# Performance work log

Hardware: AMD Instinct MI355X
Metric: run time of the kernel (lower is better)

## Reference

```python
import jax, jax.numpy as jnp
import numpy as np


def _conv(x, w):
    # stride-2, pad-1, 3x3 conv, NCHW activations, HWIO kernel
    return jax.lax.conv_general_dilated(
        x, w, (2, 2), [(1, 1), (1, 1)],
        dimension_numbers=('NCHW', 'HWIO', 'NCHW'))


def setup_inputs() -> dict:
    key = jax.random.key(0)
    ks = iter(jax.random.split(key, 40))
    def rn(shape, scale=1.0):
        return jax.random.normal(next(ks), shape, jnp.float32) * scale
    d = {}
    d['img'] = rn((64, 3, 128, 128))
    d['qst'] = rn((64, 128))
    d['conv_w0'] = rn((3, 3, 3, 24), 1.0 / np.sqrt(3 * 9))
    for i in (1, 2, 3):
        d['conv_w%d' % i] = rn((3, 3, 24, 24), 1.0 / np.sqrt(24 * 9))
    for i in range(4):
        d['bn_s%d' % i] = jax.random.uniform(next(ks), (24,), jnp.float32, 0.5, 1.5)
        d['bn_b%d' % i] = rn((24,), 0.1)
    d['g_w1'] = rn((180, 256), 1.0 / np.sqrt(180))
    d['g_b1'] = rn((256,), 0.01)
    for i in (2, 3, 4):
        d['g_w%d' % i] = rn((256, 256), 1.0 / np.sqrt(256))
        d['g_b%d' % i] = rn((256,), 0.01)
    d['f_w1'] = rn((256, 256), 1.0 / np.sqrt(256))
    d['f_b1'] = rn((256,), 0.01)
    d['f_w2'] = rn((256, 256), 1.0 / np.sqrt(256))
    d['f_b2'] = rn((256,), 0.01)
    d['cls_w'] = rn((256, 32), 1.0 / np.sqrt(256))
    d['cls_b'] = rn((32,), 0.01)
    return d


def reference(img, qst, conv_w0, conv_w1, conv_w2, conv_w3,
              bn_s0, bn_b0, bn_s1, bn_b1, bn_s2, bn_b2, bn_s3, bn_b3,
              g_w1, g_b1, g_w2, g_b2, g_w3, g_b3, g_w4, g_b4,
              f_w1, f_b1, f_w2, f_b2, cls_w, cls_b):
    x = img
    for w, s, b in ((conv_w0, bn_s0, bn_b0), (conv_w1, bn_s1, bn_b1),
                    (conv_w2, bn_s2, bn_b2), (conv_w3, bn_s3, bn_b3)):
        x = jax.nn.relu(_conv(x, w) * s[None, :, None, None] + b[None, :, None, None])
    N, C, H, W = x.shape  # [64, 24, 8, 8]
    # positional encoding: coords_x, coords_y in [-1,1]
    cx, cy = jnp.meshgrid(jnp.linspace(-1.0, 1.0, W), jnp.linspace(-1.0, 1.0, H))
    pos = jnp.broadcast_to(jnp.stack([cx, cy])[None], (N, 2, H, W)).astype(x.dtype)
    x = jnp.concatenate([x, pos], axis=1)              # [N, C+2, H, W]
    Cf = C + 2
    x = x.transpose(0, 2, 3, 1).reshape(N, H * W, Cf)  # [N, HW, 26]
    # RN_G first linear decomposed over concat([x_i, x_j, qst]) so the huge
    # [N, HW, HW, 2C+q] concat tensor is never materialized (same math).
    W1a, W1b, W1c = g_w1[:Cf], g_w1[Cf:2 * Cf], g_w1[2 * Cf:]
    hi = x @ W1a                      # [N, HW, 256]
    hj = x @ W1b                      # [N, HW, 256]
    hq = qst @ W1c + g_b1             # [N, 256]
    h = jax.nn.relu(hi[:, :, None, :] + hj[:, None, :, :] + hq[:, None, None, :])  # [N,HW,HW,256]
    h = jax.nn.relu(h @ g_w2 + g_b2)
    h = jax.nn.relu(h @ g_w3 + g_b3)
    h = jax.nn.relu(h @ g_w4 + g_b4)
    s = h.sum(axis=(1, 2))            # sum over all HW*HW pairs -> [N, 256]
    # RN_F (dropout is identity in eval mode)
    y = jax.nn.relu(s @ f_w1 + f_b1)
    y = jax.nn.relu(y @ f_w2 + f_b2)
    return jax.nn.log_softmax(y @ cls_w + cls_b, axis=1)
```

## Files before the change

### kernel.cpp

```cpp
#include <hip/hip_runtime.h>
#include <hip/hip_bf16.h>
#include <math.h>

typedef __bf16 bf16x8 __attribute__((ext_vector_type(8)));
typedef __bf16 bf16x4 __attribute__((ext_vector_type(4)));
typedef float  f32x4  __attribute__((ext_vector_type(4)));

#define LH 264

__device__ __host__ inline int fperm(int p) {
  return (p & 0xC0) | ((p & 0x0C) << 2) | ((p >> 2) & 0x0C) | (p & 3);
}

__global__ __launch_bounds__(256) void k1(const float* __restrict__ img, const float* __restrict__ w0,
    const float* __restrict__ bs0, const float* __restrict__ bb0,
    const float* __restrict__ g2, const float* __restrict__ g3, const float* __restrict__ g4,
    const float* __restrict__ gw1, const float* __restrict__ gb1, const float* __restrict__ qst,
    float* __restrict__ c0, __bf16* __restrict__ Wt, float* __restrict__ hq,
    float* __restrict__ sbuf) {
  __shared__ __align__(16) float smem[8224];
  const int blk = blockIdx.x, t = threadIdx.x;

  if (blk < 512) {
    float* wl = smem;
    for (int i = t; i < 648; i += 256) wl[i] = w0[i];
    __syncthreads();
    const int H = 128, W = 128;
    int idx = blk * 256 + t;
    int oxh = idx & 31; int tt = idx >> 5; int oy = tt & 63; int n = tt >> 6;
    int ox0 = oxh * 2;
    float acc0[24], acc1[24];
#pragma unroll
    for (int co = 0; co < 24; ++co) { acc0[co] = 0.f; acc1[co] = 0.f; }
    for (int ci = 0; ci < 3; ++ci) {
      const float* xp = img + (size_t)(n * 3 + ci) * H * W;
#pragma unroll
      for (int ky = 0; ky < 3; ++ky) {
        int iy = 2 * oy + ky - 1;
        if (iy < 0 || iy >= H) continue;
        const float* row = xp + (size_t)iy * W;
        int ixb = 2 * ox0 - 1;
        float in[7];
#pragma unroll
        for (int u = 0; u < 7; ++u) {
          int ix = ixb + u;
          in[u] = (ix >= 0 && ix < W) ? row[ix] : 0.f;
        }
#pragma unroll
        for (int kx = 0; kx < 3; ++kx) {
          const float* wp = &wl[((ky * 3 + kx) * 3 + ci) * 24];
          float v0 = in[kx], v1 = in[kx + 2];
#pragma unroll
          for (int co = 0; co < 24; ++co) {
            float wv = wp[co];
            acc0[co] += v0 * wv;
            acc1[co] += v1 * wv;
          }
        }
      }
    }
    float* yp = c0 + ((size_t)((n * 64 + oy) * 64) + ox0) * 24;
#pragma unroll
    for (int v = 0; v < 6; ++v) {
      f32x4 o;
#pragma unroll
      for (int j = 0; j < 4; ++j) {
        int co = v * 4 + j;
        o[j] = fmaxf(acc0[co] * bs0[co] + bb0[co], 0.f);
      }
      *(f32x4*)(yp + v * 4) = o;
    }
#pragma unroll
    for (int v = 0; v < 6; ++v) {
      f32x4 o;
#pragma unroll
      for (int j = 0; j < 4; ++j) {
        int co = v * 4 + j;
        o[j] = fmaxf(acc1[co] * bs0[co] + bb0[co], 0.f);
      }
      *(f32x4*)(yp + 24 + v * 4) = o;
    }
  } else if (blk < 536) {
    float* tile = smem;
    const int lb = blk - 512;
    const int l = lb >> 3, ks = lb & 7;
    const float* src = (l == 0) ? g2 : (l == 1) ? g3 : g4;
    for (int kk = 0; kk < 32; ++kk) tile[kk * 257 + t] = src[(ks * 32 + kk) * 256 + t];
    __syncthreads();
    const int q = t & 3, nb = t >> 2;
    __bf16* out = Wt + (size_t)(l * 8 + ks) * 8192;
#pragma unroll
    for (int i = 0; i < 4; ++i) {
      int nn = i * 64 + nb;
      int fsel = (l < 2) ? fperm(nn) : nn;
      bf16x8 v;
#pragma unroll
      for (int j = 0; j < 8; ++j) v[j] = (__bf16)tile[(q * 8 + j) * 257 + fsel];
      *(bf16x8*)&out[nn * 32 + q * 8] = v;
    }
  } else {
    float* qs = smem;
    const int n = blk - 536;
    sbuf[n * 256 + t] = 0.f;
    if (t < 128) qs[t] = qst[n * 128 + t];
    __syncthreads();
    float a = gb1[t];
    for (int c = 0; c < 128; ++c) a += qs[c] * gw1[(52 + c) * 256 + t];
    hq[n * 256 + t] = a;
  }
}

__global__ __launch_bounds__(256) void conv1_k(const float* __restrict__ x, const float* __restrict__ w,
                                               const float* __restrict__ sc, const float* __restrict__ bi,
                                               float* __restrict__ y) {
  __shared__ __align__(16) float wl[5184];
  const int t = threadIdx.x;
  for (int i = t; i < 5184; i += 256) wl[i] = w[i];
  __syncthreads();
  int idx = blockIdx.x * 256 + t;
  int ox = idx & 31, oy = (idx >> 5) & 31, n = idx >> 10;
  f32x4 acc4[6];
#pragma unroll
  for (int v = 0; v < 6; ++v) acc4[v] = (f32x4){0.f, 0.f, 0.f, 0.f};
  const float* xb = x + (size_t)n * 4096 * 24;
#pragma unroll
  for (int ky = 0; ky < 3; ++ky) {
    int iy = 2 * oy + ky - 1;
    if (iy < 0 || iy >= 64) continue;
#pragma unroll
    for (int kx = 0; kx < 3; ++kx) {
      int ix = 2 * ox + kx - 1;
      if (ix < 0 || ix >= 64) continue;
      const float* xp = xb + (size_t)(iy * 64 + ix) * 24;
      const float* wt = &wl[((ky * 3 + kx) * 24) * 24];
      for (int c4 = 0; c4 < 6; ++c4) {
        f32x4 xq = *(const f32x4*)(xp + c4 * 4);
        const float* wb4 = wt + (c4 * 4) * 24;
#pragma unroll
        for (int j = 0; j < 4; ++j) {
          float v = xq[j];
          const f32x4* wr = (const f32x4*)(wb4 + j * 24);
#pragma unroll
          for (int cv = 0; cv < 6; ++cv) acc4[cv] += v * wr[cv];
        }
      }
    }
  }
  float* yp = y + (size_t)idx * 24;
#pragma unroll
  for (int v = 0; v < 6; ++v) {
    f32x4 o;
#pragma unroll
    for (int j = 0; j < 4; ++j) {
      int co = v * 4 + j;
      o[j] = fmaxf(acc4[v][j] * sc[co] + bi[co], 0.f);
    }
    *(f32x4*)(yp + v * 4) = o;
  }
}

__global__ __launch_bounds__(256) void chain2_k(const float* __restrict__ c1,
    const float* __restrict__ w2, const float* __restrict__ bs2, const float* __restrict__ bb2,
    const float* __restrict__ w3, const float* __restrict__ bs3, const float* __restrict__ bb3,
    float* __restrict__ gs3) {
  __shared__ __align__(16) float sw[5184];
  __shared__ float s2[6144];
  const int n = blockIdx.x, t = threadIdx.x;
  for (int i = t; i < 5184; i += 256) sw[i] = w2[i];
  __syncthreads();
  {
    int ox = t & 15, oy = t >> 4;
    f32x4 acc4[6];
#pragma unroll
    for (int v = 0; v < 6; ++v) acc4[v] = (f32x4){0.f, 0.f, 0.f, 0.f};
    const float* xb = c1 + (size_t)n * 1024 * 24;
#pragma unroll
    for (int ky = 0; ky < 3; ++ky) {
      int iy = 2 * oy + ky - 1;
      if (iy < 0 || iy >= 32) continue;
#pragma unroll
      for (int kx = 0; kx < 3; ++kx) {
        int ix = 2 * ox + kx - 1;
        if (ix < 0 || ix >= 32) continue;
        const float* xp = xb + (size_t)(iy * 32 + ix) * 24;
        const float* wt = &sw[((ky * 3 + kx) * 24) * 24];
        for (int c4 = 0; c4 < 6; ++c4) {
          f32x4 xq = *(const f32x4*)(xp + c4 * 4);
          const float* wb4 = wt + (c4 * 4) * 24;
#pragma unroll
          for (int j = 0; j < 4; ++j) {
            float v = xq[j];
            const f32x4* wr = (const f32x4*)(wb4 + j * 24);
#pragma unroll
            for (int cv = 0; cv < 6; ++cv) acc4[cv] += v * wr[cv];
          }
        }
      }
    }
#pragma unroll
    for (int v = 0; v < 6; ++v)
#pragma unroll
      for (int j = 0; j < 4; ++j) {
        int co = v * 4 + j;
        s2[co * 256 + t] = fmaxf(acc4[v][j] * bs2[co] + bb2[co], 0.f);
      }
  }
  __syncthreads();
  for (int i = t; i < 5184; i += 256) sw[i] = w3[i];
  __syncthreads();
  {
    const int pos = t & 63, cog = t >> 6;
    const int oy = pos >> 3, ox = pos & 7;
    float acc[6];
#pragma unroll
    for (int u = 0; u < 6; ++u) acc[u] = 0.f;
    for (int ci = 0; ci < 24; ++ci) {
      const float* cp = &s2[ci * 256];
#pragma unroll
      for (int ky = 0; ky < 3; ++ky) {
        int iy = 2 * oy + ky - 1;
        if (iy < 0 || iy >= 16) continue;
#pragma unroll
        for (int kx = 0; kx < 3; ++kx) {
          int ix = 2 * ox + kx - 1;
          if (ix < 0 || ix >= 16) continue;
          float v = cp[iy * 16 + ix];
          const float* wp = &sw[((ky * 3 + kx) * 24 + ci) * 24 + cog * 6];
#pragma unroll
          for (int u = 0; u < 6; ++u) acc[u] += v * wp[u];
        }
      }
    }
#pragma unroll
    for (int u = 0; u < 6; ++u) {
      int co = cog * 6 + u;
      gs3[(size_t)n * 1536 + co * 64 + pos] = fmaxf(acc[u] * bs3[co] + bb3[co], 0.f);
    }
  }
}

__global__ __launch_bounds__(256) void embed_k(const float* __restrict__ gs3,
    const float* __restrict__ gw1, float* __restrict__ hi, float* __restrict__ hj) {
  __shared__ float s3l[1536];
  const int b = blockIdx.x, t = threadIdx.x;
  const int n = b >> 2, pg = b & 3;
  for (int i = t; i < 1536; i += 256) s3l[i] = gs3[(size_t)n * 1536 + i];
  float wa[26], wb[26];
#pragma unroll
  for (int c = 0; c < 26; ++c) {
    wa[c] = gw1[c * 256 + t];
    wb[c] = gw1[(26 + c) * 256 + t];
  }
  __syncthreads();
  for (int p = pg * 16; p < pg * 16 + 16; ++p) {
    float a = 0.f, bv = 0.f;
#pragma unroll
    for (int c = 0; c < 24; ++c) {
      float v = s3l[c * 64 + p];
      a += v * wa[c];
      bv += v * wb[c];
    }
    float cx = -1.f + (2.f / 7.f) * (float)(p & 7);
    float cy = -1.f + (2.f / 7.f) * (float)(p >> 3);
    a += cx * wa[24] + cy * wa[25];
    bv += cx * wb[24] + cy * wb[25];
    hi[(size_t)(n * 64 + p) * 256 + t] = a;
    hj[(size_t)(n * 64 + p) * 256 + t] = bv;
  }
}

__global__ __launch_bounds__(256, 2)
void g_fused(const float* __restrict__ hi, const float* __restrict__ hj,
             const float* __restrict__ hq, const __bf16* __restrict__ Wt,
             const float* __restrict__ b2, const float* __restrict__ b3,
             const float* __restrict__ b4, float* __restrict__ s_out) {
  const int blk = blockIdx.x;
  const int n = blk >> 5, ib = blk & 31;
  const int tid = threadIdx.x;
  const int wave = tid >> 6, lane = tid & 63;
  const int q = lane >> 4, lr = lane & 15;

  __shared__ __align__(16) __bf16 Hs[128 * LH];

  const int half = lane >> 5, m = lane & 31;
  const int cb = m * 8;
  float4 hqA = *(const float4*)(hq + (size_t)n * 256 + cb);
  float4 hqB = *(const float4*)(hq + (size_t)n * 256 + cb + 4);
  float4 hiA = *(const float4*)(hi + (size_t)(n * 64 + ib * 2 + half) * 256 + cb);
  float4 hiB = *(const float4*)(hi + (size_t)(n * 64 + ib * 2 + half) * 256 + cb + 4);
  float hh[8];
  hh[0] = hiA.x + hqA.x; hh[1] = hiA.y + hqA.y; hh[2] = hiA.z + hqA.z; hh[3] = hiA.w + hqA.w;
  hh[4] = hiB.x + hqB.x; hh[5] = hiB.y + hqB.y; hh[6] = hiB.z + hqB.z; hh[7] = hiB.w + hqB.w;

  float bias2[4];
#pragma unroll
  for (int c = 0; c < 4; ++c) bias2[c] = b4[wave * 64 + lr + c * 16];

  const float* hjb = hj + (size_t)n * 64 * 256;
#pragma unroll
  for (int it = 0; it < 16; ++it) {
    int j = it * 4 + wave;
    float4 va = *(const float4*)(hjb + j * 256 + cb);
    float4 vb = *(const float4*)(hjb + j * 256 + cb + 4);
    bf16x8 o;
    o[0] = (__bf16)fmaxf(va.x + hh[0], 0.f);
    o[1] = (__bf16)fmaxf(va.y + hh[1], 0.f);
    o[2] = (__bf16)fmaxf(va.z + hh[2], 0.f);
    o[3] = (__bf16)fmaxf(va.w + hh[3], 0.f);
    o[4] = (__bf16)fmaxf(vb.x + hh[4], 0.f);
    o[5] = (__bf16)fmaxf(vb.y + hh[5], 0.f);
    o[6] = (__bf16)fmaxf(vb.z + hh[6], 0.f);
    o[7] = (__bf16)fmaxf(vb.w + hh[7], 0.f);
    *(bf16x8*)&Hs[(size_t)(half * 64 + j) * LH + cb] = o;
  }
  __syncthreads();

  const __bf16* Bp = Wt + (size_t)wave * 2048 + lr * 32 + q * 8;
  const int colv = wave * 64 + q * 16;

  for (int l = 0; l < 2; ++l) {
    const __bf16* Bl = Bp + (size_t)l * 65536;
    const float* bb = (l == 0) ? b2 : b3;
    f32x4 bv[4];
#pragma unroll
    for (int c = 0; c < 4; ++c)
      bv[c] = *(const f32x4*)(bb + colv + c * 4);

    f32x4 acc[8][4];
#pragma unroll
    for (int r = 0; r < 8; ++r)
#pragma unroll
      for (int c = 0; c < 4; ++c) acc[r][c] = (f32x4){0.f, 0.f, 0.f, 0.f};

    for (int ks = 0; ks < 8; ++ks) {
      bf16x8 b[4];
#pragma unroll
      for (int c = 0; c < 4; ++c)
        b[c] = *(const bf16x8*)&Bl[ks * 8192 + c * 512];
      bf16x8 a[8];
#pragma unroll
      for (int r = 0; r < 8; ++r)
        a[r] = *(const bf16x8*)&Hs[(size_t)(r * 16 + lr) * LH + ks * 32 + q * 8];
#pragma unroll
      for (int r = 0; r < 8; ++r)
#pragma unroll
        for (int c = 0; c < 4; ++c)
          acc[r][c] = __builtin_amdgcn_mfma_f32_16x16x32_bf16(b[c], a[r], acc[r][c], 0, 0, 0);
    }

    __syncthreads();
#pragma unroll
    for (int r = 0; r < 8; ++r) {
      bf16x8 oA, oB;
#pragma unroll
      for (int c = 0; c < 2; ++c)
#pragma unroll
        for (int reg = 0; reg < 4; ++reg)
          oA[c * 4 + reg] = (__bf16)fmaxf(acc[r][c][reg] + bv[c][reg], 0.f);
#pragma unroll
      for (int c = 2; c < 4; ++c)
#pragma unroll
        for (int reg = 0; reg < 4; ++reg)
          oB[(c - 2) * 4 + reg] = (__bf16)fmaxf(acc[r][c][reg] + bv[c][reg], 0.f);
      __bf16* wp = &Hs[(size_t)(r * 16 + lr) * LH + colv];
      *(bf16x8*)wp = oA;
      *(bf16x8*)(wp + 8) = oB;
    }
    __syncthreads();
  }

  {
    const __bf16* Bl = Bp + (size_t)2 * 65536;
    f32x4 acc[8][4];
#pragma unroll
    for (int r = 0; r < 8; ++r)
#pragma unroll
      for (int c = 0; c < 4; ++c) acc[r][c] = (f32x4){0.f, 0.f, 0.f, 0.f};

    for (int ks = 0; ks < 8; ++ks) {
      bf16x8 b[4];
#pragma unroll
      for (int c = 0; c < 4; ++c)
        b[c] = *(const bf16x8*)&Bl[ks * 8192 + c * 512];
      bf16x8 a[8];
#pragma unroll
      for (int r = 0; r < 8; ++r)
        a[r] = *(const bf16x8*)&Hs[(size_t)(r * 16 + lr) * LH + ks * 32 + q * 8];
#pragma unroll
      for (int r = 0; r < 8; ++r)
#pragma unroll
        for (int c = 0; c < 4; ++c)
          acc[r][c] = __builtin_amdgcn_mfma_f32_16x16x32_bf16(a[r], b[c], acc[r][c], 0, 0, 0);
    }

#pragma unroll
    for (int c = 0; c < 4; ++c) {
      float cs = 0.f;
#pragma unroll
      for (int r = 0; r < 8; ++r)
#pragma unroll
        for (int reg = 0; reg < 4; ++reg)
          cs += fmaxf(acc[r][c][reg] + bias2[c], 0.f);
      cs += __shfl_xor(cs, 16);
      cs += __shfl_xor(cs, 32);
      if (q == 0) atomicAdd(&s_out[n * 256 + wave * 64 + lr + c * 16], cs);
    }
  }
}

__global__ void f_net(const float* __restrict__ s, const float* __restrict__ fw1,
                      const float* __restrict__ fb1, const float* __restrict__ fw2,
                      const float* __restrict__ fb2, const float* __restrict__ cw,
                      const float* __restrict__ cb, float* __restrict__ out) {
  int n = blockIdx.x, t = threadIdx.x;
  __shared__ float buf[256], buf2[256], zs[32];
  buf[t] = s[n * 256 + t];
  __syncthreads();
  float a0 = 0.f, a1 = 0.f, a2 = 0.f, a3 = 0.f;
  for (int c = 0; c < 256; c += 4) {
    a0 += buf[c]     * fw1[c * 256 + t];
    a1 += buf[c + 1] * fw1[(c + 1) * 256 + t];
    a2 += buf[c + 2] * fw1[(c + 2) * 256 + t];
    a3 += buf[c + 3] * fw1[(c + 3) * 256 + t];
  }
  float a = fmaxf(fb1[t] + ((a0 + a1) + (a2 + a3)), 0.f);
  buf2[t] = a;
  __syncthreads();
  float y0 = 0.f, y1 = 0.f, y2 = 0.f, y3 = 0.f;
  for (int c = 0; c < 256; c += 4) {
    y0 += buf2[c]     * fw2[c * 256 + t];
    y1 += buf2[c + 1] * fw2[(c + 1) * 256 + t];
    y2 += buf2[c + 2] * fw2[(c + 2) * 256 + t];
    y3 += buf2[c + 3] * fw2[(c + 3) * 256 + t];
  }
  float y = fmaxf(fb2[t] + ((y0 + y1) + (y2 + y3)), 0.f);
  __syncthreads();
  buf[t] = y;
  __syncthreads();
  float z = 0.f;
  if (t < 32) {
    float z0 = 0.f, z1 = 0.f, z2 = 0.f, z3 = 0.f;
    for (int c = 0; c < 256; c += 4) {
      z0 += buf[c]     * cw[c * 32 + t];
      z1 += buf[c + 1] * cw[(c + 1) * 32 + t];
      z2 += buf[c + 2] * cw[(c + 2) * 32 + t];
      z3 += buf[c + 3] * cw[(c + 3) * 32 + t];
    }
    z = cb[t] + ((z0 + z1) + (z2 + z3));
    zs[t] = z;
  }
  __syncthreads();
  if (t < 32) {
    float m = -1e30f;
    for (int c = 0; c < 32; ++c) m = fmaxf(m, zs[c]);
    float se = 0.f;
    for (int c = 0; c < 32; ++c) se += expf(zs[c] - m);
    out[n * 32 + t] = z - m - logf(se);
  }
}

extern "C" void kernel_launch(void* const* d_in, const int* in_sizes, int n_in,
                              void* d_out, int out_size, void* d_ws, size_t ws_size,
                              hipStream_t stream) {
  const float* img  = (const float*)d_in[0];
  const float* qst  = (const float*)d_in[1];
  const float* w0   = (const float*)d_in[2];
  const float* w1   = (const float*)d_in[3];
  const float* w2   = (const float*)d_in[4];
  const float* w3   = (const float*)d_in[5];
  const float* bs0  = (const float*)d_in[6];
  const float* bb0  = (const float*)d_in[7];
  const float* bs1  = (const float*)d_in[8];
  const float* bb1  = (const float*)d_in[9];
  const float* bs2  = (const float*)d_in[10];
  const float* bb2  = (const float*)d_in[11];
  const float* bs3  = (const float*)d_in[12];
  const float* bb3  = (const float*)d_in[13];
  const float* gw1  = (const float*)d_in[14];
  const float* gb1  = (const float*)d_in[15];
  const float* gw2  = (const float*)d_in[16];
  const float* gb2  = (const float*)d_in[17];
  const float* gw3  = (const float*)d_in[18];
  const float* gb3  = (const float*)d_in[19];
  const float* gw4  = (const float*)d_in[20];
  const float* gb4  = (const float*)d_in[21];
  const float* fw1  = (const float*)d_in[22];
  const float* fb1  = (const float*)d_in[23];
  const float* fw2  = (const float*)d_in[24];
  const float* fb2  = (const float*)d_in[25];
  const float* cw   = (const float*)d_in[26];
  const float* cb   = (const float*)d_in[27];

  char* ws = (char*)d_ws;
  float* c0 = (float*)(ws + 0);
  float* c1 = (float*)(ws + 25165824);
  __bf16* Wt  = (__bf16*)(ws + 31457280);
  float*  hqb = (float*)(ws + 31850496);
  float*  sbuf = (float*)(ws + 31916032);
  float*  hi  = (float*)(ws + 0);
  float*  hj  = (float*)(ws + 4194304);
  float*  gs3 = (float*)(ws + 8388608);

  k1<<<600, 256, 0, stream>>>(img, w0, bs0, bb0, gw2, gw3, gw4, gw1, gb1, qst,
                              c0, Wt, hqb, sbuf);
  conv1_k<<<256, 256, 0, stream>>>(c0, w1, bs1, bb1, c1);
  chain2_k<<<64, 256, 0, stream>>>(c1, w2, bs2, bb2, w3, bs3, bb3, gs3);
  embed_k<<<256, 256, 0, stream>>>(gs3, gw1, hi, hj);
  g_fused<<<2048, 256, 0, stream>>>(hi, hj, hqb, Wt, gb2, gb3, gb4, sbuf);
  f_net<<<64, 256, 0, stream>>>(sbuf, fw1, fb1, fw2, fb2, cw, cb, (float*)d_out);
}
```

Baseline: 313.6 us.

## Fuse embed into conv chain, hoist conv loads, prefetch B fragments in g_fused

Several independent changes. The conv kernels now load all input taps for a row up front, with zero-fill for padding instead of continue branches, so global loads are issued together before the FMAs. The embedding step (hi/hj projection) is folded into chain2_k, so the gs3 intermediate and one kernel launch go away; each of the 64 blocks now handles all 64 positions instead of 256 blocks handling 16 each. In g_fused the B fragments are software-prefetched one k-step ahead, the k loop is fully unrolled, and the MFMA issue is wrapped in s_setprio. Risks: higher register pressure, and less parallelism in the fused embed stage.

New measurement: 577.7 us. +84.2%, slower.

```diff
diff --git a/kernel.cpp b/kernel.cpp
--- a/kernel.cpp
+++ b/kernel.cpp
@@ -34,22 +34,24 @@
     for (int co = 0; co < 24; ++co) { acc0[co] = 0.f; acc1[co] = 0.f; }
     for (int ci = 0; ci < 3; ++ci) {
       const float* xp = img + (size_t)(n * 3 + ci) * H * W;
+      float in[3][7];
 #pragma unroll
       for (int ky = 0; ky < 3; ++ky) {
         int iy = 2 * oy + ky - 1;
-        if (iy < 0 || iy >= H) continue;
+        bool yok = (iy >= 0) && (iy < H);
         const float* row = xp + (size_t)iy * W;
-        int ixb = 2 * ox0 - 1;
-        float in[7];
 #pragma unroll
         for (int u = 0; u < 7; ++u) {
-          int ix = ixb + u;
-          in[u] = (ix >= 0 && ix < W) ? row[ix] : 0.f;
+          int ix = 2 * ox0 - 1 + u;
+          in[ky][u] = (yok && ix >= 0 && ix < W) ? row[ix] : 0.f;
         }
+      }
+#pragma unroll
+      for (int ky = 0; ky < 3; ++ky)
 #pragma unroll
         for (int kx = 0; kx < 3; ++kx) {
           const float* wp = &wl[((ky * 3 + kx) * 3 + ci) * 24];
-          float v0 = in[kx], v1 = in[kx + 2];
+          float v0 = in[ky][kx], v1 = in[ky][kx + 2];
 #pragma unroll
           for (int co = 0; co < 24; ++co) {
             float wv = wp[co];
@@ -57,7 +59,6 @@
             acc1[co] += v1 * wv;
           }
         }
-      }
     }
     float* yp = c0 + ((size_t)((n * 64 + oy) * 64) + ox0) * 24;
 #pragma unroll
@@ -123,22 +124,29 @@
 #pragma unroll
   for (int v = 0; v < 6; ++v) acc4[v] = (f32x4){0.f, 0.f, 0.f, 0.f};
   const float* xb = x + (size_t)n * 4096 * 24;
+  const f32x4 zero4 = (f32x4){0.f, 0.f, 0.f, 0.f};
 #pragma unroll
   for (int ky = 0; ky < 3; ++ky) {
     int iy = 2 * oy + ky - 1;
     if (iy < 0 || iy >= 64) continue;
+    f32x4 xin[3][6];
 #pragma unroll
     for (int kx = 0; kx < 3; ++kx) {
       int ix = 2 * ox + kx - 1;
-      if (ix < 0 || ix >= 64) continue;
+      bool ok = (ix >= 0) && (ix < 64);
       const float* xp = xb + (size_t)(iy * 64 + ix) * 24;
+#pragma unroll
+      for (int c4 = 0; c4 < 6; ++c4)
+        xin[kx][c4] = ok ? *(const f32x4*)(xp + c4 * 4) : zero4;
+    }
+#pragma unroll
+    for (int kx = 0; kx < 3; ++kx) {
       const float* wt = &wl[((ky * 3 + kx) * 24) * 24];
       for (int c4 = 0; c4 < 6; ++c4) {
-        f32x4 xq = *(const f32x4*)(xp + c4 * 4);
         const float* wb4 = wt + (c4 * 4) * 24;
 #pragma unroll
         for (int j = 0; j < 4; ++j) {
-          float v = xq[j];
+          float v = xin[kx][c4][j];
           const f32x4* wr = (const f32x4*)(wb4 + j * 24);
 #pragma unroll
           for (int cv = 0; cv < 6; ++cv) acc4[cv] += v * wr[cv];
@@ -162,9 +170,10 @@
 __global__ __launch_bounds__(256) void chain2_k(const float* __restrict__ c1,
     const float* __restrict__ w2, const float* __restrict__ bs2, const float* __restrict__ bb2,
     const float* __restrict__ w3, const float* __restrict__ bs3, const float* __restrict__ bb3,
-    float* __restrict__ gs3) {
+    const float* __restrict__ gw1, float* __restrict__ hi, float* __restrict__ hj) {
   __shared__ __align__(16) float sw[5184];
   __shared__ float s2[6144];
+  __shared__ float s3[1536];
   const int n = blockIdx.x, t = threadIdx.x;
   for (int i = t; i < 5184; i += 256) sw[i] = w2[i];
   __syncthreads();
@@ -174,22 +183,29 @@
 #pragma unroll
     for (int v = 0; v < 6; ++v) acc4[v] = (f32x4){0.f, 0.f, 0.f, 0.f};
     const float* xb = c1 + (size_t)n * 1024 * 24;
+    const f32x4 zero4 = (f32x4){0.f, 0.f, 0.f, 0.f};
 #pragma unroll
     for (int ky = 0; ky < 3; ++ky) {
       int iy = 2 * oy + ky - 1;
       if (iy < 0 || iy >= 32) continue;
+      f32x4 xin[3][6];
 #pragma unroll
       for (int kx = 0; kx < 3; ++kx) {
         int ix = 2 * ox + kx - 1;
-        if (ix < 0 || ix >= 32) continue;
+        bool ok = (ix >= 0) && (ix < 32);
         const float* xp = xb + (size_t)(iy * 32 + ix) * 24;
+#pragma unroll
+        for (int c4 = 0; c4 < 6; ++c4)
+          xin[kx][c4] = ok ? *(const f32x4*)(xp + c4 * 4) : zero4;
+      }
+#pragma unroll
+      for (int kx = 0; kx < 3; ++kx) {
         const float* wt = &sw[((ky * 3 + kx) * 24) * 24];
         for (int c4 = 0; c4 < 6; ++c4) {
-          f32x4 xq = *(const f32x4*)(xp + c4 * 4);
           const float* wb4 = wt + (c4 * 4) * 24;
 #pragma unroll
           for (int j = 0; j < 4; ++j) {
-            float v = xq[j];
+            float v = xin[kx][c4][j];
             const f32x4* wr = (const f32x4*)(wb4 + j * 24);
 #pragma unroll
             for (int cv = 0; cv < 6; ++cv) acc4[cv] += v * wr[cv];
@@ -234,17 +250,9 @@
 #pragma unroll
     for (int u = 0; u < 6; ++u) {
       int co = cog * 6 + u;
-      gs3[(size_t)n * 1536 + co * 64 + pos] = fmaxf(acc[u] * bs3[co] + bb3[co], 0.f);
-    }
-  }
-}
-
-__global__ __launch_bounds__(256) void embed_k(const float* __restrict__ gs3,
-    const float* __restrict__ gw1, float* __restrict__ hi, float* __restrict__ hj) {
-  __shared__ float s3l[1536];
-  const int b = blockIdx.x, t = threadIdx.x;
-  const int n = b >> 2, pg = b & 3;
-  for (int i = t; i < 1536; i += 256) s3l[i] = gs3[(size_t)n * 1536 + i];
+      s3[co * 64 + pos] = fmaxf(acc[u] * bs3[co] + bb3[co], 0.f);
+    }
+  }
   float wa[26], wb[26];
 #pragma unroll
   for (int c = 0; c < 26; ++c) {
@@ -252,20 +260,20 @@
     wb[c] = gw1[(26 + c) * 256 + t];
   }
   __syncthreads();
-  for (int p = pg * 16; p < pg * 16 + 16; ++p) {
-    float a = 0.f, bv = 0.f;
+  for (int p = 0; p < 64; ++p) {
+    float a = 0.f, b = 0.f;
 #pragma unroll
     for (int c = 0; c < 24; ++c) {
-      float v = s3l[c * 64 + p];
+      float v = s3[c * 64 + p];
       a += v * wa[c];
-      bv += v * wb[c];
+      b += v * wb[c];
     }
     float cx = -1.f + (2.f / 7.f) * (float)(p & 7);
     float cy = -1.f + (2.f / 7.f) * (float)(p >> 3);
     a += cx * wa[24] + cy * wa[25];
-    bv += cx * wb[24] + cy * wb[25];
+    b += cx * wb[24] + cy * wb[25];
     hi[(size_t)(n * 64 + p) * 256 + t] = a;
-    hj[(size_t)(n * 64 + p) * 256 + t] = bv;
+    hj[(size_t)(n * 64 + p) * 256 + t] = b;
   }
 }
 
@@ -332,20 +340,29 @@
 #pragma unroll
       for (int c = 0; c < 4; ++c) acc[r][c] = (f32x4){0.f, 0.f, 0.f, 0.f};
 
+    bf16x8 bnxt[4];
+#pragma unroll
+    for (int c = 0; c < 4; ++c) bnxt[c] = *(const bf16x8*)&Bl[c * 512];
+#pragma unroll
     for (int ks = 0; ks < 8; ++ks) {
-      bf16x8 b[4];
-#pragma unroll
-      for (int c = 0; c < 4; ++c)
-        b[c] = *(const bf16x8*)&Bl[ks * 8192 + c * 512];
+      bf16x8 bcur[4];
+#pragma unroll
+      for (int c = 0; c < 4; ++c) bcur[c] = bnxt[c];
+      if (ks < 7) {
+#pragma unroll
+        for (int c = 0; c < 4; ++c) bnxt[c] = *(const bf16x8*)&Bl[(ks + 1) * 8192 + c * 512];
+      }
       bf16x8 a[8];
 #pragma unroll
       for (int r = 0; r < 8; ++r)
         a[r] = *(const bf16x8*)&Hs[(size_t)(r * 16 + lr) * LH + ks * 32 + q * 8];
+      __builtin_amdgcn_s_setprio(1);
 #pragma unroll
       for (int r = 0; r < 8; ++r)
 #pragma unroll
         for (int c = 0; c < 4; ++c)
-          acc[r][c] = __builtin_amdgcn_mfma_f32_16x16x32_bf16(b[c], a[r], acc[r][c], 0, 0, 0);
+          acc[r][c] = __builtin_amdgcn_mfma_f32_16x16x32_bf16(bcur[c], a[r], acc[r][c], 0, 0, 0);
+      __builtin_amdgcn_s_setprio(0);
     }
 
     __syncthreads();
@@ -377,20 +394,29 @@
 #pragma unroll
       for (int c = 0; c < 4; ++c) acc[r][c] = (f32x4){0.f, 0.f, 0.f, 0.f};
 
+    bf16x8 bnxt[4];
+#pragma unroll
+    for (int c = 0; c < 4; ++c) bnxt[c] = *(const bf16x8*)&Bl[c * 512];
+#pragma unroll
     for (int ks = 0; ks < 8; ++ks) {
-      bf16x8 b[4];
-#pragma unroll
-      for (int c = 0; c < 4; ++c)
-        b[c] = *(const bf16x8*)&Bl[ks * 8192 + c * 512];
+      bf16x8 bcur[4];
+#pragma unroll
+      for (int c = 0; c < 4; ++c) bcur[c] = bnxt[c];
+      if (ks < 7) {
+#pragma unroll
+        for (int c = 0; c < 4; ++c) bnxt[c] = *(const bf16x8*)&Bl[(ks + 1) * 8192 + c * 512];
+      }
       bf16x8 a[8];
 #pragma unroll
       for (int r = 0; r < 8; ++r)
         a[r] = *(const bf16x8*)&Hs[(size_t)(r * 16 + lr) * LH + ks * 32 + q * 8];
+      __builtin_amdgcn_s_setprio(1);
 #pragma unroll
       for (int r = 0; r < 8; ++r)
 #pragma unroll
         for (int c = 0; c < 4; ++c)
-          acc[r][c] = __builtin_amdgcn_mfma_f32_16x16x32_bf16(a[r], b[c], acc[r][c], 0, 0, 0);
+          acc[r][c] = __builtin_amdgcn_mfma_f32_16x16x32_bf16(a[r], bcur[c], acc[r][c], 0, 0, 0);
+      __builtin_amdgcn_s_setprio(0);
     }
 
 #pragma unroll
@@ -451,11 +477,11 @@
   }
   __syncthreads();
   if (t < 32) {
-    float m = -1e30f;
-    for (int c = 0; c < 32; ++c) m = fmaxf(m, zs[c]);
+    float mx = -1e30f;
+    for (int c = 0; c < 32; ++c) mx = fmaxf(mx, zs[c]);
     float se = 0.f;
-    for (int c = 0; c < 32; ++c) se += expf(zs[c] - m);
-    out[n * 32 + t] = z - m - logf(se);
+    for (int c = 0; c < 32; ++c) se += expf(zs[c] - mx);
+    out[n * 32 + t] = z - mx - logf(se);
   }
 }
 
@@ -499,13 +525,11 @@
   float*  sbuf = (float*)(ws + 31916032);
   float*  hi  = (float*)(ws + 0);
   float*  hj  = (float*)(ws + 4194304);
-  float*  gs3 = (float*)(ws + 8388608);
 
   k1<<<600, 256, 0, stream>>>(img, w0, bs0, bb0, gw2, gw3, gw4, gw1, gb1, qst,
                               c0, Wt, hqb, sbuf);
   conv1_k<<<256, 256, 0, stream>>>(c0, w1, bs1, bb1, c1);
-  chain2_k<<<64, 256, 0, stream>>>(c1, w2, bs2, bb2, w3, bs3, bb3, gs3);
-  embed_k<<<256, 256, 0, stream>>>(gs3, gw1, hi, hj);
+  chain2_k<<<64, 256, 0, stream>>>(c1, w2, bs2, bb2, w3, bs3, bb3, gw1, hi, hj);
   g_fused<<<2048, 256, 0, stream>>>(hi, hj, hqb, Wt, gb2, gb3, gb4, sbuf);
   f_net<<<64, 256, 0, stream>>>(sbuf, fw1, fb1, fw2, fb2, cw, cb, (float*)d_out);
 }
```
